# Kernel tuning notes

Measured on AMD Instinct MI355X. Metric: run time of the kernel, lower is better.

Reference implementation:

```python
import jax, jax.numpy as jnp
from jax import lax
import numpy as np
import math

B, T, D, H, DFF, L = 64, 351, 512, 8, 1024, 3
DK = D // H
SQRT_DIM = math.sqrt(D)


def setup_inputs() -> dict:
    key = jax.random.key(0)
    ks = jax.random.split(key, 32)
    s = 0.02
    n = lambda k, shape, sc=s: jax.random.normal(k, shape, jnp.float32) * sc
    inp = {
        'x': jax.random.normal(ks[0], (B, T, D), jnp.float32),
        'mask': jax.random.normal(ks[1], (B, T, D), jnp.float32),  # float stream: used as pos_embedding inside attention
        'pos_emb': n(ks[2], (L, T, D)),           # Encoder.pos_embedding_{1,2,3}
        'Wq': n(ks[3], (L, D, D)), 'bq': jnp.zeros((L, D), jnp.float32),
        'Wk': n(ks[4], (L, D, D)), 'bk': jnp.zeros((L, D), jnp.float32),
        'Wv': n(ks[5], (L, D, D)), 'bv': jnp.zeros((L, D), jnp.float32),
        'Wp': n(ks[6], (L, D, D)),                 # pos_proj, no bias
        'u_bias': n(ks[7], (L, H, DK)), 'v_bias': n(ks[8], (L, H, DK)),
        'Wo': n(ks[9], (L, D, D)), 'bo': jnp.zeros((L, D), jnp.float32),
        'ln1_a': jnp.ones((L, D), jnp.float32), 'ln1_b': jnp.zeros((L, D), jnp.float32),
        'ln2_a': jnp.ones((L, D), jnp.float32), 'ln2_b': jnp.zeros((L, D), jnp.float32),
        'W1': n(ks[10], (L, DFF, D)), 'b1': jnp.zeros((L, DFF), jnp.float32),   # conv1d k=1
        'W2': n(ks[11], (L, D, DFF, 3)), 'b2': jnp.zeros((L, D), jnp.float32),  # conv1d k=3 pad=1
        'fn_a': jnp.ones((D,), jnp.float32), 'fn_b': jnp.zeros((D,), jnp.float32),
    }
    return inp


def layernorm(x, a, b, eps=1e-6):
    # torch: a*(x-mean)/(std+eps)+b with unbiased std (Bessel, n-1)
    mean = x.mean(-1, keepdims=True)
    xc = x - mean
    std = jnp.sqrt((xc * xc).sum(-1, keepdims=True) / (x.shape[-1] - 1))
    return a * xc / (std + eps) + b


def rel_shift(ps):
    # Transformer-XL relative shift via pad+reshape
    b, h, t1, t2 = ps.shape
    p = jnp.pad(ps, ((0, 0), (0, 0), (0, 0), (1, 0)))
    p = p.reshape(b, h, t2 + 1, t1)
    return p[:, :, 1:].reshape(b, h, t1, t2)


def attention(xn, pe, Wq, bq, Wk, bk, Wv, bv, Wp, u, v, Wo, bo):
    b, t, _ = xn.shape
    q = (xn @ Wq.T + bq).reshape(b, t, H, DK)
    k = (xn @ Wk.T + bk).reshape(b, t, H, DK)
    val = (xn @ Wv.T + bv).reshape(b, t, H, DK)
    p = (pe @ Wp.T).reshape(b, t, H, DK)
    content = jnp.einsum('bqhd,bkhd->bhqk', q + u, k)
    pos = rel_shift(jnp.einsum('bqhd,bkhd->bhqk', q + v, p))
    attn = jax.nn.softmax((content + pos) / SQRT_DIM, axis=-1)  # mask=None path; dropout inactive (eval)
    ctx = jnp.einsum('bhqk,bkhd->bqhd', attn, val).reshape(b, t, D)
    return ctx @ Wo.T + bo


def reference(x, mask, pos_emb, Wq, bq, Wk, bk, Wv, bv, Wp, u_bias, v_bias, Wo, bo,
              ln1_a, ln1_b, ln2_a, ln2_b, W1, b1, W2, b2, fn_a, fn_b):
    for i in range(L):
        x = x + pos_emb[i][None]
        # sublayer 0: pre-LN relative MHA with residual (stride_num[i]==1)
        xn = layernorm(x, ln1_a[i], ln1_b[i])
        x = x + attention(xn, mask, Wq[i], bq[i], Wk[i], bk[i], Wv[i], bv[i],
                          Wp[i], u_bias[i], v_bias[i], Wo[i], bo[i])
        # sublayer 1: pre-LN conv FFN (k=1 conv -> ReLU -> k=3 conv, pad 1, stride 1)
        xn = layernorm(x, ln2_a[i], ln2_b[i])
        h = jax.nn.relu(jnp.einsum('btd,fd->btf', xn, W1[i]) + b1[i])
        y = lax.conv_general_dilated(h.transpose(0, 2, 1), W2[i], (1,), [(1, 1)],
                                     dimension_numbers=('NCH', 'OIH', 'NCH'))
        x = x + (y + b2[i][None, :, None]).transpose(0, 2, 1)
    return layernorm(x, fn_a, fn_b)
```

## Files before the change

kernel.cpp:

```cpp
#include <hip/hip_runtime.h>
#include <hip/hip_bf16.h>

typedef __hip_bfloat16 bf16;
typedef __attribute__((ext_vector_type(8))) short short8;
typedef __attribute__((ext_vector_type(4))) float f32x4;

constexpr int BB  = 64;
constexpr int TT  = 351;
constexpr int DD  = 512;
constexpr int HH  = 8;
constexpr int DK  = 64;
constexpr int FF  = 1024;
constexpr int LL  = 3;
constexpr int MT  = BB * TT;
constexpr int TD  = TT * DD;

constexpr int QT  = 32;
constexpr int NQT = (TT + QT - 1) / QT;

constexpr size_t LW      = 3407872;
constexpr size_t OFF_QKV = 0;
constexpr size_t OFF_P   = 786432;
constexpr size_t OFF_O   = 1048576;
constexpr size_t OFF_W1  = 1310720;
constexpr size_t OFF_W2  = 1835008;

__device__ __forceinline__ float us2f(unsigned short u) {
    union { unsigned int i; float f; } c; c.i = ((unsigned int)u) << 16; return c.f;
}
__device__ __forceinline__ float bf2f(bf16 h) { return __bfloat162float(h); }
__device__ __forceinline__ bf16  f2bf(float f) { return __float2bfloat16(f); }
__device__ __forceinline__ float ldin(const void* p, size_t i, bool f32) {
    return f32 ? ((const float*)p)[i] : bf2f(((const bf16*)p)[i]);
}
__device__ __forceinline__ unsigned short f2us(float f) {
    bf16 h = f2bf(f); return *reinterpret_cast<unsigned short*>(&h);
}

__global__ void detect_kernel(const unsigned short* ln1a, int* flag) {
    if (threadIdx.x == 0 && blockIdx.x == 0)
        *flag = (ln1a[0] == 0) ? 1 : 0;
}

__global__ __launch_bounds__(256) void cvt_kernel(
    const void* __restrict__ src, size_t S, size_t slstride,
    bf16* __restrict__ dst, size_t doff, int nl, int mode,
    const int* __restrict__ dflag)
{
    const bool f32 = (*dflag != 0);
    size_t i = (size_t)blockIdx.x * 256 + threadIdx.x;
    size_t total = (size_t)nl * S;
    if (i >= total) return;
    size_t l = i / S, e = i - l * S;
    size_t se;
    if (mode == 1) {
        size_t j = e >> 19;
        size_t nf = e & ((1u << 19) - 1);
        size_t n = nf >> 10, f = nf & 1023;
        se = n * 3072 + f * 3 + j;
    } else se = e;
    dst[doff + l * LW + e] = f2bf(ldin(src, l * slstride + se, f32));
}

__global__ __launch_bounds__(256) void addpos_kernel(
    const void* __restrict__ xin, const void* __restrict__ pos, size_t posoff,
    float* __restrict__ xf, int init, const int* __restrict__ dflag)
{
    const bool f32 = (*dflag != 0);
    int i = blockIdx.x * 256 + threadIdx.x;
    if (i >= MT * DD) return;
    int td = i % TD;
    float p = ldin(pos, posoff + td, f32);
    if (init) xf[i] = ldin(xin, i, f32) + p;
    else      xf[i] += p;
}

__global__ __launch_bounds__(256) void ln_kernel(
    const float* __restrict__ xf, const void* __restrict__ ga, size_t gaoff,
    const void* __restrict__ gb, size_t gboff,
    void* __restrict__ out, int final_o, const int* __restrict__ dflag)
{
    const bool f32 = (*dflag != 0);
    __shared__ float red[256];
    const int row = blockIdx.x;
    const int tid = threadIdx.x;
    const float* xr = xf + (size_t)row * DD;
    float x0 = xr[tid], x1 = xr[tid + 256];

    red[tid] = x0 + x1;
    __syncthreads();
    for (int o = 128; o > 0; o >>= 1) {
        if (tid < o) red[tid] += red[tid + o];
        __syncthreads();
    }
    float mean = red[0] * (1.0f / 512.0f);
    __syncthreads();
    float c0 = x0 - mean, c1 = x1 - mean;
    red[tid] = c0 * c0 + c1 * c1;
    __syncthreads();
    for (int o = 128; o > 0; o >>= 1) {
        if (tid < o) red[tid] += red[tid + o];
        __syncthreads();
    }
    float stdv = sqrtf(red[0] * (1.0f / 511.0f));
    float inv = 1.0f / (stdv + 1e-6f);
    float v0 = ldin(ga, gaoff + tid,       f32) * c0 * inv + ldin(gb, gboff + tid,       f32);
    float v1 = ldin(ga, gaoff + tid + 256, f32) * c1 * inv + ldin(gb, gboff + tid + 256, f32);
    if (final_o && f32) {
        float* orow = (float*)out + (size_t)row * DD;
        orow[tid] = v0; orow[tid + 256] = v1;
    } else {
        bf16* orow = (bf16*)out + (size_t)row * DD;
        orow[tid] = f2bf(v0); orow[tid + 256] = f2bf(v1);
    }
}

__global__ __launch_bounds__(256) void mgemm_kernel(
    const void* __restrict__ A, size_t aoff, int a_ext,
    const bf16* __restrict__ W,
    const void* __restrict__ b0, const void* __restrict__ b1p,
    const void* __restrict__ b2p, size_t boff,
    void* __restrict__ outp, int M, int N, int K, int mode, int chN,
    const int* __restrict__ dflag)
{
    const bool f32 = (*dflag != 0);
    const bool a32 = a_ext && f32;
    __shared__ unsigned short As[128][40];
    __shared__ unsigned short Bs[128][40];
    const int tid = threadIdx.x;
    const int n0 = blockIdx.x * 128, m0 = blockIdx.y * 128;

    const int lane = tid & 63, wv = tid >> 6;
    const int wm = wv >> 1, wn = wv & 1;
    const int q = lane >> 4, lm = lane & 15;

    f32x4 acc[4][4] = {};

    for (int k0 = 0; k0 < K; k0 += 32) {
        #pragma unroll
        for (int part = 0; part < 2; ++part) {
            int idx = part * 256 + tid;
            int row = idx >> 2;
            int seg = (idx & 3) * 8;
            int grow = m0 + row; if (grow >= M) grow = M - 1;
            if (a32) {
                const float* ap = (const float*)A + aoff + (size_t)grow * K + k0 + seg;
                union { unsigned short us[8]; int4 v; } t;
                #pragma unroll
                for (int e = 0; e < 8; ++e) t.us[e] = f2us(ap[e]);
                *(int4*)&As[row][seg] = t.v;
            } else {
                *(int4*)&As[row][seg] =
                    *(const int4*)((const bf16*)A + aoff + (size_t)grow * K + k0 + seg);
            }
            *(int4*)&Bs[row][seg] =
                *(const int4*)(W + (size_t)(n0 + row) * K + k0 + seg);
        }
        __syncthreads();
        short8 af[4], bfv[4];
        #pragma unroll
        for (int i = 0; i < 4; ++i) af[i]  = *(const short8*)&As[wm * 64 + i * 16 + lm][q * 8];
        #pragma unroll
        for (int j = 0; j < 4; ++j) bfv[j] = *(const short8*)&Bs[wn * 64 + j * 16 + lm][q * 8];
        #pragma unroll
        for (int i = 0; i < 4; ++i)
            #pragma unroll
            for (int j = 0; j < 4; ++j)
                acc[i][j] = __builtin_amdgcn_mfma_f32_16x16x32_bf16(af[i], bfv[j], acc[i][j], 0, 0, 0);
        __syncthreads();
    }

    #pragma unroll
    for (int i = 0; i < 4; ++i) {
        #pragma unroll
        for (int j = 0; j < 4; ++j) {
            #pragma unroll
            for (int r = 0; r < 4; ++r) {
                int m = m0 + wm * 64 + i * 16 + q * 4 + r;
                if (m >= M) continue;
                int n = n0 + wn * 64 + j * 16 + lm;
                float c = acc[i][j][r];
                if (mode == 0) {
                    int which = n >> 9;
                    int nn = n & 511;
                    const void* bp = which == 0 ? b0 : (which == 1 ? b1p : b2p);
                    if (bp) c += ldin(bp, boff + nn, f32);
                    int b = m / TT, t = m - b * TT;
                    int h = nn >> 6, dk = nn & 63;
                    ((bf16*)outp)[(size_t)which * chN +
                                  ((((size_t)b * HH + h) * TT + t) * DK) + dk] = f2bf(c);
                } else if (mode == 1) {
                    if (b0) c += ldin(b0, boff + n, f32);
                    ((bf16*)outp)[(size_t)m * N + n] = f2bf(fmaxf(c, 0.0f));
                } else {
                    if (b0) c += ldin(b0, boff + n, f32);
                    ((float*)outp)[(size_t)m * DD + n] += c;
                }
            }
        }
    }
}

__global__ __launch_bounds__(256) void mconv_kernel(
    const bf16* __restrict__ Hb, const bf16* __restrict__ Wc,
    const void* __restrict__ bias, size_t boff,
    float* __restrict__ xf, int M, const int* __restrict__ dflag)
{
    const bool f32 = (*dflag != 0);
    __shared__ unsigned short As[128][40];
    __shared__ unsigned short Bs[128][40];
    const int tid = threadIdx.x;
    const int n0 = blockIdx.x * 128, m0 = blockIdx.y * 128;

    const int lane = tid & 63, wv = tid >> 6;
    const int wm = wv >> 1, wn = wv & 1;
    const int q = lane >> 4, lm = lane & 15;

    int rowP[2], segP[2], mloadP[2], trowP[2];
    bool inrP[2];
    #pragma unroll
    for (int part = 0; part < 2; ++part) {
        int idx = part * 256 + tid;
        rowP[part] = idx >> 2;
        segP[part] = (idx & 3) * 8;
        int mrow = m0 + rowP[part];
        inrP[part] = mrow < M;
        int mload = inrP[part] ? mrow : (M - 1);
        mloadP[part] = mload;
        trowP[part] = mload % TT;
    }

    f32x4 acc[4][4] = {};

    for (int j = 0; j < 3; ++j) {
        for (int k0 = 0; k0 < FF; k0 += 32) {
            #pragma unroll
            for (int part = 0; part < 2; ++part) {
                int row = rowP[part], seg = segP[part];
                int ts = trowP[part] + j - 1;
                bool valid = inrP[part] && ts >= 0 && ts < TT;
                if (valid) {
                    *(int4*)&As[row][seg] =
                        *(const int4*)(Hb + (size_t)(mloadP[part] + j - 1) * FF + k0 + seg);
                } else {
                    int4 z = {0, 0, 0, 0};
                    *(int4*)&As[row][seg] = z;
                }
                *(int4*)&Bs[row][seg] =
                    *(const int4*)(Wc + (size_t)j * 524288 + (size_t)(n0 + row) * FF + k0 + seg);
            }
            __syncthreads();
            short8 af[4], bfv[4];
            #pragma unroll
            for (int i = 0; i < 4; ++i) af[i]  = *(const short8*)&As[wm * 64 + i * 16 + lm][q * 8];
            #pragma unroll
            for (int jj = 0; jj < 4; ++jj) bfv[jj] = *(const short8*)&Bs[wn * 64 + jj * 16 + lm][q * 8];
            #pragma unroll
            for (int i = 0; i < 4; ++i)
                #pragma unroll
                for (int jj = 0; jj < 4; ++jj)
                    acc[i][jj] = __builtin_amdgcn_mfma_f32_16x16x32_bf16(af[i], bfv[jj], acc[i][jj], 0, 0, 0);
            __syncthreads();
        }
    }

    #pragma unroll
    for (int i = 0; i < 4; ++i) {
        #pragma unroll
        for (int jj = 0; jj < 4; ++jj) {
            #pragma unroll
            for (int r = 0; r < 4; ++r) {
                int m = m0 + wm * 64 + i * 16 + q * 4 + r;
                if (m >= M) continue;
                int n = n0 + wn * 64 + jj * 16 + lm;
                xf[(size_t)m * DD + n] += acc[i][jj][r] + ldin(bias, boff + n, f32);
            }
        }
    }
}

__global__ __launch_bounds__(256) void attn_kernel(
    const bf16* __restrict__ Q, const bf16* __restrict__ Kb,
    const bf16* __restrict__ V, const bf16* __restrict__ P,
    const void* __restrict__ ubias, const void* __restrict__ vbias, size_t uvoff,
    bf16* __restrict__ ctx, const int* __restrict__ dflag)
{
    const bool f32 = (*dflag != 0);
    const int d  = blockIdx.x + NQT * (blockIdx.y + HH * blockIdx.z);
    const int rr = d % (8 * NQT);
    const int g  = (d / (8 * NQT)) * 8 + (rr & 7);
    const int t  = rr >> 3;
    const int b  = g >> 3;
    const int h  = g & 7;
    const int q0 = t * QT;

    const int tid  = threadIdx.x;
    const int lane = tid & 63;
    const int wv   = tid >> 6;
    const int lm   = lane & 15;
    const int q8   = lane >> 4;

    __shared__ __align__(16) char sbuf[46080];
    float (*S)[356] = reinterpret_cast<float(*)[356]>(sbuf);
    unsigned short (*Vt)[360] = reinterpret_cast<unsigned short(*)[360]>(sbuf);

    __shared__ __align__(16) unsigned short Abf[QT][360];
    __shared__ __align__(16) unsigned short qu[32][72];
    __shared__ __align__(16) unsigned short qv[48][72];

    const size_t base = (((size_t)b * HH + h) * TT) * DK;
    const float scale = 0.04419417382415922f;

    for (int i = tid; i < 48 * 64; i += 256) {
        int q = i >> 6, dd = i & 63;
        int qrow = q0 + q;
        float qq = (qrow < TT) ? bf2f(Q[base + (size_t)qrow * DK + dd]) : 0.0f;
        float vb = ldin(vbias, uvoff + h * DK + dd, f32);
        qv[q][dd] = (qrow < TT) ? f2us((qq + vb) * scale) : (unsigned short)0;
        if (q < 32) {
            float ub = ldin(ubias, uvoff + h * DK + dd, f32);
            qu[q][dd] = f2us((qq + ub) * scale);
        }
    }
    __syncthreads();

    short8 kv0[6], kv1[6], pv0[6], pv1[6];
    #pragma unroll
    for (int it = 0; it < 6; ++it) {
        int jt = wv + it * 4;
        int kr = jt * 16 + lm; if (kr > TT - 1) kr = TT - 1;
        const short8* kp = (const short8*)(Kb + base + (size_t)kr * DK + q8 * 8);
        const short8* pp = (const short8*)(P  + base + (size_t)kr * DK + q8 * 8);
        kv0[it] = kp[0]; kv1[it] = kp[4];
        pv0[it] = pp[0]; pv1[it] = pp[4];
    }

    {
        short8 af0a = *(const short8*)&qu[lm][q8 * 8];
        short8 af0b = *(const short8*)&qu[lm][32 + q8 * 8];
        short8 af1a = *(const short8*)&qu[16 + lm][q8 * 8];
        short8 af1b = *(const short8*)&qu[16 + lm][32 + q8 * 8];
        #pragma unroll
        for (int it = 0; it < 6; ++it) {
            int jt = wv + it * 4;
            if (jt >= 22) break;
            f32x4 a0 = {}, a1 = {};
            a0 = __builtin_amdgcn_mfma_f32_16x16x32_bf16(af0a, kv0[it], a0, 0, 0, 0);
            a0 = __builtin_amdgcn_mfma_f32_16x16x32_bf16(af0b, kv1[it], a0, 0, 0, 0);
            a1 = __builtin_amdgcn_mfma_f32_16x16x32_bf16(af1a, kv0[it], a1, 0, 0, 0);
            a1 = __builtin_amdgcn_mfma_f32_16x16x32_bf16(af1b, kv1[it], a1, 0, 0, 0);
            int col = jt * 16 + lm;
            #pragma unroll
            for (int r = 0; r < 4; ++r) {
                S[q8 * 4 + r][col]      = a0[r];
                S[16 + q8 * 4 + r][col] = a1[r];
            }
        }
    }
    __syncthreads();

    {
        short8 af[3][2];
        #pragma unroll
        for (int i = 0; i < 3; ++i) {
            af[i][0] = *(const short8*)&qv[i * 16 + lm][q8 * 8];
            af[i][1] = *(const short8*)&qv[i * 16 + lm][32 + q8 * 8];
        }
        #pragma unroll
        for (int it = 0; it < 6; ++it) {
            int jt = wv + it * 4;
            if (jt >= 22) break;
            f32x4 acc[3] = {};
            #pragma unroll
            for (int i = 0; i < 3; ++i) {
                acc[i] = __builtin_amdgcn_mfma_f32_16x16x32_bf16(af[i][0], pv0[it], acc[i], 0, 0, 0);
                acc[i] = __builtin_amdgcn_mfma_f32_16x16x32_bf16(af[i][1], pv1[it], acc[i], 0, 0, 0);
            }
            int j = jt * 16 + lm;
            if (j < TT) {
                #pragma unroll
                for (int i = 0; i < 3; ++i) {
                    #pragma unroll
                    for (int r = 0; r < 4; ++r) {
                        int rl = i * 16 + q8 * 4 + r;
                        int rg = q0 + rl;
                        int cb  = (j + rg < TT - 1) ? 1 : 0;
                        int row = rl - cb;
                        int col = j + rg - (TT - 1) + cb * TT;
                        if (row >= 0 && row < QT) S[row][col] += acc[i][r];
                    }
                }
            }
        }
    }
    __syncthreads();

    {
        const int row = tid >> 3, k0 = tid & 7;
        float* Sr = S[row];
        float m = -1e30f;
        for (int k = k0; k < TT; k += 8) m = fmaxf(m, Sr[k]);
        #pragma unroll
        for (int msk = 1; msk < 8; msk <<= 1) m = fmaxf(m, __shfl_xor(m, msk));
        float sum = 0.0f;
        for (int k = k0; k < TT; k += 8) {
            float e = __expf(Sr[k] - m);
            Sr[k] = e;
            sum += e;
        }
        #pragma unroll
        for (int msk = 1; msk < 8; msk <<= 1) sum += __shfl_xor(sum, msk);
        float rinv = 1.0f / sum;
        for (int k = k0; k < 360; k += 8)
            Abf[row][k] = (k < TT) ? f2us(Sr[k] * rinv) : (unsigned short)0;
    }
    __syncthreads();

    {
        short8 v0[6], v1[6];
        #pragma unroll
        for (int it = 0; it < 6; ++it) {
            int idx = it * 256 + tid;
            int p2 = idx >> 3, dsg = idx & 7;
            if (p2 > 175) p2 = 175;
            int k0r = p2 * 2;
            v0[it] = *(const short8*)(V + base + (size_t)k0r * DK + dsg * 8);
            int k1 = (k0r + 1 < TT) ? (k0r + 1) : k0r;
            v1[it] = *(const short8*)(V + base + (size_t)k1 * DK + dsg * 8);
        }
        #pragma unroll
        for (int it = 0; it < 6; ++it) {
            int idx = it * 256 + tid;
            if (idx < 176 * 8) {
                int p2 = idx >> 3, dsg = idx & 7;
                int k0r = p2 * 2;
                const bool hasv1 = (k0r + 1 < TT);
                #pragma unroll
                for (int e = 0; e < 8; ++e) {
                    unsigned int pk = (unsigned int)(unsigned short)v0[it][e];
                    if (hasv1) pk |= ((unsigned int)(unsigned short)v1[it][e]) << 16;
                    *(unsigned int*)&Vt[dsg * 8 + e][k0r] = pk;
                }
            }
        }
    }
    __syncthreads();

    {
        f32x4 a0 = {}, a1 = {};
        for (int ks = 0; ks < 11; ++ks) {
            short8 bv  = *(const short8*)&Vt[wv * 16 + lm][ks * 32 + q8 * 8];
            short8 av0 = *(const short8*)&Abf[lm][ks * 32 + q8 * 8];
            short8 av1 = *(const short8*)&Abf[16 + lm][ks * 32 + q8 * 8];
            a0 = __builtin_amdgcn_mfma_f32_16x16x32_bf16(av0, bv, a0, 0, 0, 0);
            a1 = __builtin_amdgcn_mfma_f32_16x16x32_bf16(av1, bv, a1, 0, 0, 0);
        }
        const int dd = wv * 16 + lm;
        #pragma unroll
        for (int r = 0; r < 4; ++r) {
            int qrow = q0 + q8 * 4 + r;
            if (qrow < TT)
                ctx[((size_t)b * TT + qrow) * DD + h * DK + dd] = f2bf(a0[r]);
            qrow = q0 + 16 + q8 * 4 + r;
            if (qrow < TT)
                ctx[((size_t)b * TT + qrow) * DD + h * DK + dd] = f2bf(a1[r]);
        }
    }
}

extern "C" void kernel_launch(void* const* d_in, const int* in_sizes, int n_in,
                              void* d_out, int out_size, void* d_ws, size_t ws_size,
                              hipStream_t stream)
{
    (void)in_sizes; (void)n_in; (void)out_size;
    const void* x    = d_in[0];
    const void* mask = d_in[1];
    const void* pos  = d_in[2];
    const void* Wq   = d_in[3];
    const void* bq   = d_in[4];
    const void* Wk   = d_in[5];
    const void* bk   = d_in[6];
    const void* Wv   = d_in[7];
    const void* bv   = d_in[8];
    const void* Wp   = d_in[9];
    const void* ub   = d_in[10];
    const void* vbi  = d_in[11];
    const void* Wo   = d_in[12];
    const void* bo   = d_in[13];
    const void* l1a  = d_in[14];
    const void* l1b  = d_in[15];
    const void* l2a  = d_in[16];
    const void* l2b  = d_in[17];
    const void* W1   = d_in[18];
    const void* b1   = d_in[19];
    const void* W2   = d_in[20];
    const void* b2   = d_in[21];
    const void* fa   = d_in[22];
    const void* fb   = d_in[23];

    const size_t exf = (size_t)MT * DD;
    char* w = (char*)d_ws;
    int*   dflag = (int*)w;
    float* xf = (float*)(w + 256);
    bf16*  xn = (bf16*)(w + 256 + exf * 4);
    bf16*  sc = (bf16*)(w + 256 + exf * 6);
    bf16*  wbuf = (bf16*)d_out;

    const size_t fixed = 256 + exf * 6;
    int cha = 8;
    if      (ws_size >= fixed + (size_t)4 * 64 * TT * DD * 2) cha = 64;
    else if (ws_size >= fixed + (size_t)4 * 32 * TT * DD * 2) cha = 32;
    else if (ws_size >= fixed + (size_t)4 * 16 * TT * DD * 2) cha = 16;
    const int nca = BB / cha;
    const int ma  = cha * TT;
    const int chf = (cha * 2 > 64) ? 64 : cha * 2;
    const int ncf = BB / chf;
    const int mf  = chf * TT;
    const int chN = ma * DD;

    bf16* qc = sc;
    bf16* pc = sc + (size_t)3 * chN;
    bf16* hb = sc;

    dim3 blk(256);
    dim3 g_ep((MT * DD + 255) / 256);
    dim3 g_ln(MT);
    dim3 g_qkv(12, (ma + 127) / 128);
    dim3 g_p(4, (ma + 127) / 128);
    dim3 g_attn(NQT, HH, cha);
    dim3 g_o(4, (MT + 127) / 128);
    dim3 g_f1(8, (mf + 127) / 128);
    dim3 g_cv(4, (mf + 127) / 128);

    detect_kernel<<<dim3(1), dim3(64), 0, stream>>>((const unsigned short*)l1a, dflag);

    auto cvt = [&](const void* src, size_t S, size_t doff, int mode) {
        dim3 g((unsigned)(((size_t)3 * S + 255) / 256));
        cvt_kernel<<<g, blk, 0, stream>>>(src, S, S, wbuf, doff, 3, mode, dflag);
    };
    cvt(Wq, 262144, OFF_QKV,          0);
    cvt(Wk, 262144, OFF_QKV + 262144, 0);
    cvt(Wv, 262144, OFF_QKV + 524288, 0);
    cvt(Wp, 262144, OFF_P,            0);
    cvt(Wo, 262144, OFF_O,            0);
    cvt(W1, 524288, OFF_W1,           0);
    cvt(W2, 1572864, OFF_W2,          1);

    for (int l = 0; l < LL; ++l) {
        const bf16* wl = wbuf + (size_t)l * LW;
        addpos_kernel<<<g_ep, blk, 0, stream>>>(x, pos, (size_t)l * TD, xf, l == 0, dflag);
        ln_kernel<<<g_ln, blk, 0, stream>>>(xf, l1a, (size_t)l * DD, l1b, (size_t)l * DD, xn, 0, dflag);
        for (int c = 0; c < nca; ++c) {
            bf16* xnc = xn + (size_t)c * ma * DD;
            mgemm_kernel<<<g_qkv, blk, 0, stream>>>(xnc, 0, 0, wl + OFF_QKV,
                bq, bk, bv, (size_t)l * DD, qc, ma, 1536, DD, 0, chN, dflag);
            mgemm_kernel<<<g_p, blk, 0, stream>>>(mask, (size_t)c * ma * DD, 1, wl + OFF_P,
                nullptr, nullptr, nullptr, 0, pc, ma, DD, DD, 0, 0, dflag);
            attn_kernel<<<g_attn, blk, 0, stream>>>(qc, qc + chN, qc + 2 * (size_t)chN, pc,
                ub, vbi, (size_t)l * HH * DK, xnc, dflag);
        }
        mgemm_kernel<<<g_o, blk, 0, stream>>>(xn, 0, 0, wl + OFF_O,
            bo, nullptr, nullptr, (size_t)l * DD, xf, MT, DD, DD, 2, 0, dflag);
        ln_kernel<<<g_ln, blk, 0, stream>>>(xf, l2a, (size_t)l * DD, l2b, (size_t)l * DD, xn, 0, dflag);
        for (int c = 0; c < ncf; ++c) {
            mgemm_kernel<<<g_f1, blk, 0, stream>>>(xn + (size_t)c * mf * DD, 0, 0, wl + OFF_W1,
                b1, nullptr, nullptr, (size_t)l * FF, hb, mf, FF, DD, 1, 0, dflag);
            mconv_kernel<<<g_cv, blk, 0, stream>>>(hb, wl + OFF_W2,
                b2, (size_t)l * DD, xf + (size_t)c * mf * DD, mf, dflag);
        }
    }
    ln_kernel<<<g_ln, blk, 0, stream>>>(xf, fa, 0, fb, 0, d_out, 1, dflag);
}
```

Baseline: 2.630 ms.

## Prefetch V before softmax, register-cache scores, swizzle transposed V in LDS

Issues the global loads of V into registers before the softmax phase so their latency overlaps the softmax instead of stalling after it. The softmax row values are held in a 44-entry register array rather than reread from shared memory each pass. The transposed V tile in LDS gets an XOR swizzle to reduce bank conflicts on both the write and the MFMA read. Launch bounds are raised to request two blocks per SM, which together with the larger register footprint risks spills.

```diff
diff --git a/kernel.cpp b/kernel.cpp
--- a/kernel.cpp
+++ b/kernel.cpp
@@ -279,7 +279,7 @@
     }
 }
 
-__global__ __launch_bounds__(256) void attn_kernel(
+__global__ __launch_bounds__(256, 2) void attn_kernel(
     const bf16* __restrict__ Q, const bf16* __restrict__ Kb,
     const bf16* __restrict__ V, const bf16* __restrict__ P,
     const void* __restrict__ ubias, const void* __restrict__ vbias, size_t uvoff,
@@ -302,7 +302,6 @@
 
     __shared__ __align__(16) char sbuf[46080];
     float (*S)[356] = reinterpret_cast<float(*)[356]>(sbuf);
-    unsigned short (*Vt)[360] = reinterpret_cast<unsigned short(*)[360]>(sbuf);
 
     __shared__ __align__(16) unsigned short Abf[QT][360];
     __shared__ __align__(16) unsigned short qu[32][72];
@@ -395,39 +394,52 @@
     }
     __syncthreads();
 
+    short8 v0r[6], v1r[6];
+    #pragma unroll
+    for (int it = 0; it < 6; ++it) {
+        int idx = it * 256 + tid;
+        int p2 = idx >> 3, dsg = idx & 7;
+        if (p2 > 175) p2 = 175;
+        int k0r = p2 * 2;
+        v0r[it] = *(const short8*)(V + base + (size_t)k0r * DK + dsg * 8);
+        int k1 = (k0r + 1 < TT) ? (k0r + 1) : k0r;
+        v1r[it] = *(const short8*)(V + base + (size_t)k1 * DK + dsg * 8);
+    }
     {
         const int row = tid >> 3, k0 = tid & 7;
-        float* Sr = S[row];
+        const float* Sr = S[row];
+        float sv[44];
+        #pragma unroll
+        for (int i = 0; i < 44; ++i) {
+            int k = k0 + 8 * i;
+            sv[i] = (k < TT) ? Sr[k] : -1e30f;
+        }
         float m = -1e30f;
-        for (int k = k0; k < TT; k += 8) m = fmaxf(m, Sr[k]);
+        #pragma unroll
+        for (int i = 0; i < 44; ++i) m = fmaxf(m, sv[i]);
         #pragma unroll
         for (int msk = 1; msk < 8; msk <<= 1) m = fmaxf(m, __shfl_xor(m, msk));
         float sum = 0.0f;
-        for (int k = k0; k < TT; k += 8) {
-            float e = __expf(Sr[k] - m);
-            Sr[k] = e;
+        #pragma unroll
+        for (int i = 0; i < 44; ++i) {
+            float e = __expf(sv[i] - m);
+            sv[i] = e;
             sum += e;
         }
         #pragma unroll
         for (int msk = 1; msk < 8; msk <<= 1) sum += __shfl_xor(sum, msk);
         float rinv = 1.0f / sum;
-        for (int k = k0; k < 360; k += 8)
-            Abf[row][k] = (k < TT) ? f2us(Sr[k] * rinv) : (unsigned short)0;
+        #pragma unroll
+        for (int i = 0; i < 45; ++i) {
+            int k = k0 + 8 * i;
+            if (k < 360)
+                Abf[row][k] = (k < TT && i < 44) ? f2us(sv[i] * rinv) : (unsigned short)0;
+        }
     }
     __syncthreads();
 
     {
-        short8 v0[6], v1[6];
-        #pragma unroll
-        for (int it = 0; it < 6; ++it) {
-            int idx = it * 256 + tid;
-            int p2 = idx >> 3, dsg = idx & 7;
-            if (p2 > 175) p2 = 175;
-            int k0r = p2 * 2;
-            v0[it] = *(const short8*)(V + base + (size_t)k0r * DK + dsg * 8);
-            int k1 = (k0r + 1 < TT) ? (k0r + 1) : k0r;
-            v1[it] = *(const short8*)(V + base + (size_t)k1 * DK + dsg * 8);
-        }
+        char* vb = sbuf;
         #pragma unroll
         for (int it = 0; it < 6; ++it) {
             int idx = it * 256 + tid;
@@ -437,9 +449,10 @@
                 const bool hasv1 = (k0r + 1 < TT);
                 #pragma unroll
                 for (int e = 0; e < 8; ++e) {
-                    unsigned int pk = (unsigned int)(unsigned short)v0[it][e];
-                    if (hasv1) pk |= ((unsigned int)(unsigned short)v1[it][e]) << 16;
-                    *(unsigned int*)&Vt[dsg * 8 + e][k0r] = pk;
+                    unsigned int pk = (unsigned int)(unsigned short)v0r[it][e];
+                    if (hasv1) pk |= ((unsigned int)(unsigned short)v1r[it][e]) << 16;
+                    int off = (dsg * 8 + e) * 720 + ((k0r * 2) ^ ((dsg & 3) << 4));
+                    *(unsigned int*)(vb + off) = pk;
                 }
             }
         }
@@ -447,9 +460,13 @@
     __syncthreads();
 
     {
+        const char* vb = sbuf;
+        const int vrow = wv * 16 + lm;
+        const int rx = ((vrow >> 3) & 3) << 4;
         f32x4 a0 = {}, a1 = {};
         for (int ks = 0; ks < 11; ++ks) {
-            short8 bv  = *(const short8*)&Vt[wv * 16 + lm][ks * 32 + q8 * 8];
+            int off = vrow * 720 + ((ks * 64 + q8 * 16) ^ rx);
+            short8 bv  = *(const short8*)(vb + off);
             short8 av0 = *(const short8*)&Abf[lm][ks * 32 + q8 * 8];
             short8 av1 = *(const short8*)&Abf[16 + lm][ks * 32 + q8 * 8];
             a0 = __builtin_amdgcn_mfma_f32_16x16x32_bf16(av0, bv, a0, 0, 0, 0);
```

New measurement: 2.451 ms. -6.8%, faster.

## Write V pre-transposed from QKV GEMM and shrink attention query tile to 16

Applied to the files above, without the earlier changes.

The QKV GEMM epilogue now writes V directly in a transposed, padded [b,h,dk,t] layout, so the attention kernel no longer transposes V through shared memory and can load its MFMA B-operands straight into registers. The query tile drops from 32 to 16 rows, which cuts shared memory and adds launch_bounds occupancy hints so more blocks fit per CU. Softmax rows are held in registers with 16 lanes per row. The cost is that K and P rows are reloaded by twice as many blocks, the transposed V stores are strided, and workspace chunk sizing changes.

```diff
diff --git a/kernel.cpp b/kernel.cpp
--- a/kernel.cpp
+++ b/kernel.cpp
@@ -15,8 +15,9 @@
 constexpr int MT  = BB * TT;
 constexpr int TD  = TT * DD;
 
-constexpr int QT  = 32;
+constexpr int QT  = 16;
 constexpr int NQT = (TT + QT - 1) / QT;
+constexpr int VTS = 352;
 
 constexpr size_t LW      = 3407872;
 constexpr size_t OFF_QKV = 0;
@@ -120,7 +121,8 @@
     const bf16* __restrict__ W,
     const void* __restrict__ b0, const void* __restrict__ b1p,
     const void* __restrict__ b2p, size_t boff,
-    void* __restrict__ outp, int M, int N, int K, int mode, int chN,
+    void* __restrict__ outp, bf16* __restrict__ vt,
+    int M, int N, int K, int mode, int chN,
     const int* __restrict__ dflag)
 {
     const bool f32 = (*dflag != 0);
@@ -187,8 +189,14 @@
                     if (bp) c += ldin(bp, boff + nn, f32);
                     int b = m / TT, t = m - b * TT;
                     int h = nn >> 6, dk = nn & 63;
-                    ((bf16*)outp)[(size_t)which * chN +
-                                  ((((size_t)b * HH + h) * TT + t) * DK) + dk] = f2bf(c);
+                    if (which == 2) {
+                        size_t idxv = ((size_t)(b * HH + h) * DK + dk) * VTS + t;
+                        vt[idxv] = f2bf(c);
+                        if (t == TT - 1) vt[idxv + 1] = f2bf(0.0f);
+                    } else {
+                        ((bf16*)outp)[(size_t)which * chN +
+                                      ((((size_t)b * HH + h) * TT + t) * DK) + dk] = f2bf(c);
+                    }
                 } else if (mode == 1) {
                     if (b0) c += ldin(b0, boff + n, f32);
                     ((bf16*)outp)[(size_t)m * N + n] = f2bf(fmaxf(c, 0.0f));
@@ -279,9 +287,9 @@
     }
 }
 
-__global__ __launch_bounds__(256) void attn_kernel(
+__global__ __launch_bounds__(256, 4) void attn_kernel(
     const bf16* __restrict__ Q, const bf16* __restrict__ Kb,
-    const bf16* __restrict__ V, const bf16* __restrict__ P,
+    const bf16* __restrict__ Vt, const bf16* __restrict__ P,
     const void* __restrict__ ubias, const void* __restrict__ vbias, size_t uvoff,
     bf16* __restrict__ ctx, const int* __restrict__ dflag)
 {
@@ -300,24 +308,21 @@
     const int lm   = lane & 15;
     const int q8   = lane >> 4;
 
-    __shared__ __align__(16) char sbuf[46080];
-    float (*S)[356] = reinterpret_cast<float(*)[356]>(sbuf);
-    unsigned short (*Vt)[360] = reinterpret_cast<unsigned short(*)[360]>(sbuf);
-
-    __shared__ __align__(16) unsigned short Abf[QT][360];
-    __shared__ __align__(16) unsigned short qu[32][72];
-    __shared__ __align__(16) unsigned short qv[48][72];
+    __shared__ __align__(16) float S[QT][354];
+    __shared__ __align__(16) unsigned short Abf[QT][356];
+    __shared__ __align__(16) unsigned short qu[QT][72];
+    __shared__ __align__(16) unsigned short qv[QT + 2][72];
 
     const size_t base = (((size_t)b * HH + h) * TT) * DK;
     const float scale = 0.04419417382415922f;
 
-    for (int i = tid; i < 48 * 64; i += 256) {
+    for (int i = tid; i < (QT + 1) * 64; i += 256) {
         int q = i >> 6, dd = i & 63;
         int qrow = q0 + q;
         float qq = (qrow < TT) ? bf2f(Q[base + (size_t)qrow * DK + dd]) : 0.0f;
         float vb = ldin(vbias, uvoff + h * DK + dd, f32);
-        qv[q][dd] = (qrow < TT) ? f2us((qq + vb) * scale) : (unsigned short)0;
-        if (q < 32) {
+        qv[q][dd] = f2us((qq + vb) * scale);
+        if (q < QT) {
             float ub = ldin(ubias, uvoff + h * DK + dd, f32);
             qu[q][dd] = f2us((qq + ub) * scale);
         }
@@ -336,58 +341,53 @@
     }
 
     {
-        short8 af0a = *(const short8*)&qu[lm][q8 * 8];
-        short8 af0b = *(const short8*)&qu[lm][32 + q8 * 8];
-        short8 af1a = *(const short8*)&qu[16 + lm][q8 * 8];
-        short8 af1b = *(const short8*)&qu[16 + lm][32 + q8 * 8];
+        short8 afa = *(const short8*)&qu[lm][q8 * 8];
+        short8 afb = *(const short8*)&qu[lm][32 + q8 * 8];
         #pragma unroll
         for (int it = 0; it < 6; ++it) {
             int jt = wv + it * 4;
-            if (jt >= 22) break;
-            f32x4 a0 = {}, a1 = {};
-            a0 = __builtin_amdgcn_mfma_f32_16x16x32_bf16(af0a, kv0[it], a0, 0, 0, 0);
-            a0 = __builtin_amdgcn_mfma_f32_16x16x32_bf16(af0b, kv1[it], a0, 0, 0, 0);
-            a1 = __builtin_amdgcn_mfma_f32_16x16x32_bf16(af1a, kv0[it], a1, 0, 0, 0);
-            a1 = __builtin_amdgcn_mfma_f32_16x16x32_bf16(af1b, kv1[it], a1, 0, 0, 0);
+            if (jt >= NQT) break;
+            f32x4 a0 = {};
+            a0 = __builtin_amdgcn_mfma_f32_16x16x32_bf16(afa, kv0[it], a0, 0, 0, 0);
+            a0 = __builtin_amdgcn_mfma_f32_16x16x32_bf16(afb, kv1[it], a0, 0, 0, 0);
             int col = jt * 16 + lm;
             #pragma unroll
-            for (int r = 0; r < 4; ++r) {
-                S[q8 * 4 + r][col]      = a0[r];
-                S[16 + q8 * 4 + r][col] = a1[r];
-            }
+            for (int r = 0; r < 4; ++r)
+                S[q8 * 4 + r][col] = a0[r];
         }
     }
     __syncthreads();
 
     {
-        short8 af[3][2];
-        #pragma unroll
-        for (int i = 0; i < 3; ++i) {
-            af[i][0] = *(const short8*)&qv[i * 16 + lm][q8 * 8];
-            af[i][1] = *(const short8*)&qv[i * 16 + lm][32 + q8 * 8];
+        short8 af0a = *(const short8*)&qv[lm][q8 * 8];
+        short8 af0b = *(const short8*)&qv[lm][32 + q8 * 8];
+        short8 af1a = {}, af1b = {};
+        if (lm == 0) {
+            af1a = *(const short8*)&qv[QT][q8 * 8];
+            af1b = *(const short8*)&qv[QT][32 + q8 * 8];
         }
         #pragma unroll
         for (int it = 0; it < 6; ++it) {
             int jt = wv + it * 4;
-            if (jt >= 22) break;
-            f32x4 acc[3] = {};
-            #pragma unroll
-            for (int i = 0; i < 3; ++i) {
-                acc[i] = __builtin_amdgcn_mfma_f32_16x16x32_bf16(af[i][0], pv0[it], acc[i], 0, 0, 0);
-                acc[i] = __builtin_amdgcn_mfma_f32_16x16x32_bf16(af[i][1], pv1[it], acc[i], 0, 0, 0);
-            }
+            if (jt >= NQT) break;
+            f32x4 ac0 = {}, ac1 = {};
+            ac0 = __builtin_amdgcn_mfma_f32_16x16x32_bf16(af0a, pv0[it], ac0, 0, 0, 0);
+            ac0 = __builtin_amdgcn_mfma_f32_16x16x32_bf16(af0b, pv1[it], ac0, 0, 0, 0);
+            ac1 = __builtin_amdgcn_mfma_f32_16x16x32_bf16(af1a, pv0[it], ac1, 0, 0, 0);
+            ac1 = __builtin_amdgcn_mfma_f32_16x16x32_bf16(af1b, pv1[it], ac1, 0, 0, 0);
             int j = jt * 16 + lm;
             if (j < TT) {
                 #pragma unroll
-                for (int i = 0; i < 3; ++i) {
+                for (int i = 0; i < 2; ++i) {
                     #pragma unroll
                     for (int r = 0; r < 4; ++r) {
                         int rl = i * 16 + q8 * 4 + r;
                         int rg = q0 + rl;
+                        float v = (i == 0) ? ac0[r] : ac1[r];
                         int cb  = (j + rg < TT - 1) ? 1 : 0;
                         int row = rl - cb;
                         int col = j + rg - (TT - 1) + cb * TT;
-                        if (row >= 0 && row < QT) S[row][col] += acc[i][r];
+                        if (row >= 0 && row < QT) S[row][col] += v;
                     }
                 }
             }
@@ -395,65 +395,51 @@
     }
     __syncthreads();
 
+    const bf16* vrp = Vt + ((size_t)(b * HH + h) * DK + wv * 16 + lm) * VTS;
+    short8 bvv[11];
+    #pragma unroll
+    for (int ks = 0; ks < 11; ++ks)
+        bvv[ks] = *(const short8*)(vrp + ks * 32 + q8 * 8);
+
     {
-        const int row = tid >> 3, k0 = tid & 7;
-        float* Sr = S[row];
+        const int row = tid >> 4, k0 = tid & 15;
+        const float* Sr = S[row];
+        float sv[22];
+        #pragma unroll
+        for (int i = 0; i < 22; ++i) {
+            int k = k0 + 16 * i;
+            sv[i] = (k < TT) ? Sr[k] : -1e30f;
+        }
         float m = -1e30f;
-        for (int k = k0; k < TT; k += 8) m = fmaxf(m, Sr[k]);
-        #pragma unroll
-        for (int msk = 1; msk < 8; msk <<= 1) m = fmaxf(m, __shfl_xor(m, msk));
+        #pragma unroll
+        for (int i = 0; i < 22; ++i) m = fmaxf(m, sv[i]);
+        #pragma unroll
+        for (int msk = 1; msk < 16; msk <<= 1) m = fmaxf(m, __shfl_xor(m, msk));
         float sum = 0.0f;
-        for (int k = k0; k < TT; k += 8) {
-            float e = __expf(Sr[k] - m);
-            Sr[k] = e;
+        #pragma unroll
+        for (int i = 0; i < 22; ++i) {
+            float e = __expf(sv[i] - m);
+            sv[i] = e;
             sum += e;
         }
         #pragma unroll
-        for (int msk = 1; msk < 8; msk <<= 1) sum += __shfl_xor(sum, msk);
+        for (int msk = 1; msk < 16; msk <<= 1) sum += __shfl_xor(sum, msk);
         float rinv = 1.0f / sum;
-        for (int k = k0; k < 360; k += 8)
-            Abf[row][k] = (k < TT) ? f2us(Sr[k] * rinv) : (unsigned short)0;
+        #pragma unroll
+        for (int i = 0; i < 23; ++i) {
+            int k = k0 + 16 * i;
+            if (k < 356)
+                Abf[row][k] = (k < TT && i < 22) ? f2us(sv[i] * rinv) : (unsigned short)0;
+        }
     }
     __syncthreads();
 
     {
-        short8 v0[6], v1[6];
-        #pragma unroll
-        for (int it = 0; it < 6; ++it) {
-            int idx = it * 256 + tid;
-            int p2 = idx >> 3, dsg = idx & 7;
-            if (p2 > 175) p2 = 175;
-            int k0r = p2 * 2;
-            v0[it] = *(const short8*)(V + base + (size_t)k0r * DK + dsg * 8);
-            int k1 = (k0r + 1 < TT) ? (k0r + 1) : k0r;
-            v1[it] = *(const short8*)(V + base + (size_t)k1 * DK + dsg * 8);
-        }
-        #pragma unroll
-        for (int it = 0; it < 6; ++it) {
-            int idx = it * 256 + tid;
-            if (idx < 176 * 8) {
-                int p2 = idx >> 3, dsg = idx & 7;
-                int k0r = p2 * 2;
-                const bool hasv1 = (k0r + 1 < TT);
-                #pragma unroll
-                for (int e = 0; e < 8; ++e) {
-                    unsigned int pk = (unsigned int)(unsigned short)v0[it][e];
-                    if (hasv1) pk |= ((unsigned int)(unsigned short)v1[it][e]) << 16;
-                    *(unsigned int*)&Vt[dsg * 8 + e][k0r] = pk;
-                }
-            }
-        }
-    }
-    __syncthreads();
-
-    {
-        f32x4 a0 = {}, a1 = {};
+        f32x4 a0 = {};
+        #pragma unroll
         for (int ks = 0; ks < 11; ++ks) {
-            short8 bv  = *(const short8*)&Vt[wv * 16 + lm][ks * 32 + q8 * 8];
-            short8 av0 = *(const short8*)&Abf[lm][ks * 32 + q8 * 8];
-            short8 av1 = *(const short8*)&Abf[16 + lm][ks * 32 + q8 * 8];
-            a0 = __builtin_amdgcn_mfma_f32_16x16x32_bf16(av0, bv, a0, 0, 0, 0);
-            a1 = __builtin_amdgcn_mfma_f32_16x16x32_bf16(av1, bv, a1, 0, 0, 0);
+            short8 av = *(const short8*)&Abf[lm][ks * 32 + q8 * 8];
+            a0 = __builtin_amdgcn_mfma_f32_16x16x32_bf16(av, bvv[ks], a0, 0, 0, 0);
         }
         const int dd = wv * 16 + lm;
         #pragma unroll
@@ -461,9 +447,6 @@
             int qrow = q0 + q8 * 4 + r;
             if (qrow < TT)
                 ctx[((size_t)b * TT + qrow) * DD + h * DK + dd] = f2bf(a0[r]);
-            qrow = q0 + 16 + q8 * 4 + r;
-            if (qrow < TT)
-                ctx[((size_t)b * TT + qrow) * DD + h * DK + dd] = f2bf(a1[r]);
         }
     }
 }
@@ -506,21 +489,23 @@
     bf16*  sc = (bf16*)(w + 256 + exf * 6);
     bf16*  wbuf = (bf16*)d_out;
 
-    const size_t fixed = 256 + exf * 6;
+    const size_t fixed  = 256 + exf * 6;
+    const size_t percha = (size_t)(3 * TT * DD + HH * DK * VTS) * 2;
     int cha = 8;
-    if      (ws_size >= fixed + (size_t)4 * 64 * TT * DD * 2) cha = 64;
-    else if (ws_size >= fixed + (size_t)4 * 32 * TT * DD * 2) cha = 32;
-    else if (ws_size >= fixed + (size_t)4 * 16 * TT * DD * 2) cha = 16;
+    if      (ws_size >= fixed + 64 * percha) cha = 64;
+    else if (ws_size >= fixed + 32 * percha) cha = 32;
+    else if (ws_size >= fixed + 16 * percha) cha = 16;
     const int nca = BB / cha;
     const int ma  = cha * TT;
     const int chf = (cha * 2 > 64) ? 64 : cha * 2;
     const int ncf = BB / chf;
     const int mf  = chf * TT;
-    const int chN = ma * DD;
-
-    bf16* qc = sc;
-    bf16* pc = sc + (size_t)3 * chN;
-    bf16* hb = sc;
+    const int chN = cha * TT * DD;
+
+    bf16* qc  = sc;
+    bf16* pc  = sc + (size_t)2 * chN;
+    bf16* vtg = sc + (size_t)3 * chN;
+    bf16* hb  = sc;
 
     dim3 blk(256);
     dim3 g_ep((MT * DD + 255) / 256);
@@ -553,18 +538,18 @@
         for (int c = 0; c < nca; ++c) {
             bf16* xnc = xn + (size_t)c * ma * DD;
             mgemm_kernel<<<g_qkv, blk, 0, stream>>>(xnc, 0, 0, wl + OFF_QKV,
-                bq, bk, bv, (size_t)l * DD, qc, ma, 1536, DD, 0, chN, dflag);
+                bq, bk, bv, (size_t)l * DD, qc, vtg, ma, 1536, DD, 0, chN, dflag);
             mgemm_kernel<<<g_p, blk, 0, stream>>>(mask, (size_t)c * ma * DD, 1, wl + OFF_P,
-                nullptr, nullptr, nullptr, 0, pc, ma, DD, DD, 0, 0, dflag);
-            attn_kernel<<<g_attn, blk, 0, stream>>>(qc, qc + chN, qc + 2 * (size_t)chN, pc,
+                nullptr, nullptr, nullptr, 0, pc, nullptr, ma, DD, DD, 0, 0, dflag);
+            attn_kernel<<<g_attn, blk, 0, stream>>>(qc, qc + chN, vtg, pc,
                 ub, vbi, (size_t)l * HH * DK, xnc, dflag);
         }
         mgemm_kernel<<<g_o, blk, 0, stream>>>(xn, 0, 0, wl + OFF_O,
-            bo, nullptr, nullptr, (size_t)l * DD, xf, MT, DD, DD, 2, 0, dflag);
+            bo, nullptr, nullptr, (size_t)l * DD, xf, nullptr, MT, DD, DD, 2, 0, dflag);
         ln_kernel<<<g_ln, blk, 0, stream>>>(xf, l2a, (size_t)l * DD, l2b, (size_t)l * DD, xn, 0, dflag);
         for (int c = 0; c < ncf; ++c) {
             mgemm_kernel<<<g_f1, blk, 0, stream>>>(xn + (size_t)c * mf * DD, 0, 0, wl + OFF_W1,
-                b1, nullptr, nullptr, (size_t)l * FF, hb, mf, FF, DD, 1, 0, dflag);
+                b1, nullptr, nullptr, (size_t)l * FF, hb, nullptr, mf, FF, DD, 1, 0, dflag);
             mconv_kernel<<<g_cv, blk, 0, stream>>>(hb, wl + OFF_W2,
                 b2, (size_t)l * DD, xf + (size_t)c * mf * DD, mf, dflag);
         }
```

Result: slower. 2.950 ms (+12.2%).
